# Performance work log

Hardware: AMD Instinct MI355X
Metric: run time of the kernel (lower is better)

## Reference

```python
import jax, jax.numpy as jnp
import numpy as np

B, T, N, H = 512, 128, 128, 256


def setup_inputs() -> dict:
    key = jax.random.key(0)
    ks = jax.random.split(key, 8)
    rn = lambda k, shape, sc: (jax.random.normal(k, shape, jnp.float32) * sc)
    return {
        "data": rn(ks[0], (B, T, N), 1.0),
        "h0": jnp.zeros((B, H), jnp.float32),
        # SimpleRNNCell params: h_t = tanh(x@Wx + h@Wh + b)
        "Wx": rn(ks[1], (N, H), 0.05),
        "Wh": rn(ks[2], (H, H), 0.05),
        "b": jnp.zeros((H,), jnp.float32),
        # InputAttention: w1: Dense(T) over last dim T; w2: Dense(T) over hidden; v: Dense(1)
        "W1": rn(ks[3], (T, T), 0.05),
        "b1": jnp.zeros((T,), jnp.float32),
        "W2": rn(ks[4], (H, T), 0.05),
        "b2": jnp.zeros((T,), jnp.float32),
        "Wv": rn(ks[5], (T, 1), 0.05),
        "bv": jnp.zeros((1,), jnp.float32),
        "n": N,
    }


def reference(data, h0, Wx, Wh, b, W1, b1, W2, b2, Wv, bv, n):
    # data: (B, T, n); h0: (B, H)
    Tlen = data.shape[1]
    x_perm = jnp.swapaxes(data, 1, 2)          # (B, n, T) == Permute((2,1))(x)
    pre = x_perm @ W1 + b1                      # w1(x_perm): loop-invariant, hoisted

    def step(h, x_t):
        # SimpleRNNCell: new state used for this step's attention
        h_new = jnp.tanh(x_t @ Wx + h @ Wh + b)                 # (B, H)
        q = h_new @ W2 + b2                                      # w2(RepeatVector(n)(h)) per row -> (B, T)
        score = jnp.tanh(pre + q[:, None, :])                    # (B, n, T)
        e = score @ Wv + bv                                      # (B, n, 1)
        e = jnp.swapaxes(e, 1, 2)                                # Permute((2,1)) -> (B, 1, n)
        alpha = jax.nn.softmax(e, axis=-1)                       # softmax over n
        return h_new, alpha

    xs = jnp.swapaxes(data, 0, 1)               # (T, B, n): data[:, t, :] per step
    _, alphas = jax.lax.scan(step, h0, xs)      # (T, B, 1, n)
    # faithful to tf.reshape(alpha_seq.stack(), (-1, T, n))
    alpha_seq = alphas.reshape(-1, Tlen, n)     # (B, T, n)
    return data * alpha_seq
```

## Files before the change

kernel.cpp:

```cpp
#include <hip/hip_runtime.h>


#define C2L 2.8853900817779268f
#define L2E 1.4426950408889634f

typedef _Float16 hf;
typedef _Float16 hf2 __attribute__((ext_vector_type(2)));
typedef _Float16 hf4 __attribute__((ext_vector_type(4)));
typedef _Float16 hf8 __attribute__((ext_vector_type(8)));
typedef float f32x4 __attribute__((ext_vector_type(4)));

__device__ __forceinline__ float fast_exp2(float x){
#if __has_builtin(__builtin_amdgcn_exp2f)
  return __builtin_amdgcn_exp2f(x);
#else
  return exp2f(x);
#endif
}
__device__ __forceinline__ float fast_rcp(float x){
#if __has_builtin(__builtin_amdgcn_rcpf)
  return __builtin_amdgcn_rcpf(x);
#else
  return 1.f/x;
#endif
}

__global__ __launch_bounds__(256) void k_prep_w(const float* __restrict__ Wx,
    const float* __restrict__ W2, const float* __restrict__ W1,
    hf* __restrict__ wts){
  int tid = blockIdx.x*256 + threadIdx.x;
  if (tid < 32768){
    int n = tid >> 7, k = tid & 127;
    wts[tid] = (hf)Wx[k*256 + n];
  } else if (tid < 65536){
    int t2 = tid - 32768;
    int n = t2 >> 8, k = t2 & 255;
    wts[tid] = (hf)W2[k*128 + n];
  } else {
    int t3 = tid - 65536;
    int n = t3 >> 7, k = t3 & 127;
    wts[tid] = (hf)W1[k*128 + n];
  }
}

template<int K, int MODE>
__global__ __launch_bounds__(256) void k_gemm(const void* __restrict__ Asrc,
    const hf* __restrict__ Bt, const float* __restrict__ bias,
    float* __restrict__ Cout){
  constexpr int SA = 136;
  __shared__ alignas(16) hf As[64*SA];
  __shared__ alignas(16) hf Bs[128*SA];
  const int tid = threadIdx.x;
  const int w = tid >> 6, lane = tid & 63;
  const int c = lane & 15, q = lane >> 4;
  const int bx = blockIdx.x;
  const int col0 = (MODE==0) ? blockIdx.y*128 : 0;

  float br[8];
  #pragma unroll
  for (int ni=0; ni<8; ni++) br[ni] = bias[col0 + ni*16 + c];

  f32x4 acc[8];
  #pragma unroll
  for (int ni=0; ni<8; ni++) acc[ni] = (f32x4){0.f,0.f,0.f,0.f};

  for (int kc=0; kc<K/128; kc++){
    if (MODE == 0){
      const float* A = (const float*)Asrc + (long)bx*64*128;
      #pragma unroll
      for (int v=0; v<8; v++){
        int f4 = v*256 + tid;
        int m = f4 >> 5, k4 = (f4 & 31)*4;
        float4 d = *(const float4*)&A[m*128 + k4];
        hf4 h = {(hf)d.x,(hf)d.y,(hf)d.z,(hf)d.w};
        *(hf4*)&As[m*SA + k4] = h;
      }
    } else if (MODE == 1){
      const hf* A = (const hf*)Asrc + (long)bx*64*256;
      #pragma unroll
      for (int v=0; v<4; v++){
        int f8 = v*256 + tid;
        int m = f8 >> 4, k8 = (f8 & 15)*8;
        *(hf8*)&As[m*SA + k8] = *(const hf8*)&A[m*256 + kc*128 + k8];
      }
    } else {
      const float* A = (const float*)Asrc + (long)(bx>>1)*16384;
      const int i0 = (bx & 1)*64;
      #pragma unroll
      for (int v=0; v<8; v++){
        int f4 = v*256 + tid;
        int t = f4 >> 4, i4 = (f4 & 15)*4;
        float4 d = *(const float4*)&A[t*128 + i0 + i4];
        As[(i4+0)*SA + t] = (hf)d.x;
        As[(i4+1)*SA + t] = (hf)d.y;
        As[(i4+2)*SA + t] = (hf)d.z;
        As[(i4+3)*SA + t] = (hf)d.w;
      }
    }
    #pragma unroll
    for (int v=0; v<8; v++){
      int f8 = v*256 + tid;
      int n = f8 >> 4, k8 = (f8 & 15)*8;
      *(hf8*)&Bs[n*SA + k8] = *(const hf8*)&Bt[(col0+n)*K + kc*128 + k8];
    }
    __syncthreads();
    #pragma unroll
    for (int kk=0; kk<4; kk++){
      hf8 a = *(const hf8*)&As[(w*16 + c)*SA + kk*32 + q*8];
      #pragma unroll
      for (int ni=0; ni<8; ni++){
        hf8 b = *(const hf8*)&Bs[(ni*16 + c)*SA + kk*32 + q*8];
        acc[ni] = __builtin_amdgcn_mfma_f32_16x16x32_f16(a, b, acc[ni], 0, 0, 0);
      }
    }
    __syncthreads();
  }
  #pragma unroll
  for (int ni=0; ni<8; ni++){
    #pragma unroll
    for (int r=0; r<4; r++){
      int rloc = w*16 + q*4 + r;
      int col = col0 + ni*16 + c;
      float val = acc[ni][r] + br[ni];
      int addr;
      if (MODE == 0){
        int R = bx*64 + rloc;
        int b_ = R >> 7, t_ = R & 127;
        addr = (t_*512 + b_)*256 + col;
      } else if (MODE == 1){
        int R = bx*64 + rloc;
        addr = R*128 + col;
        val = fast_exp2(C2L*val);
      } else {
        int b_ = bx >> 1, i_ = (bx & 1)*64 + rloc;
        addr = b_*16384 + i_*128 + col;
        val = fast_exp2(C2L*val);
      }
      Cout[addr] = val;
    }
  }
}

__global__ __launch_bounds__(512, 2) void k_rnn(const float* __restrict__ h0,
    const float* __restrict__ Wh, const float* __restrict__ xw,
    hf* __restrict__ Hb){
  __shared__ alignas(16) char hs[2*8192];
  const int tid = threadIdx.x;
  const int w = tid >> 6, lane = tid & 63;
  const int c = lane & 15, q = lane >> 4;
  const int b0 = blockIdx.x * 16;
  const int w0 = w * 32;
  hf8 bw[2][8];
  #pragma unroll
  for (int nt=0; nt<2; nt++){
    #pragma unroll
    for (int kc=0; kc<8; kc++){
      #pragma unroll
      for (int e=0; e<8; e++){
        bw[nt][kc][e] = (hf)Wh[(kc*32 + q*8 + e)*256 + w0 + nt*16 + c];
      }
    }
  }
  {
    int m = tid >> 5, s8 = tid & 31;
    const float* src = &h0[(b0 + m)*256 + s8*8];
    float4 d0 = *(const float4*)&src[0];
    float4 d1 = *(const float4*)&src[4];
    hf8 hv = {(hf)d0.x,(hf)d0.y,(hf)d0.z,(hf)d0.w,
              (hf)d1.x,(hf)d1.y,(hf)d1.z,(hf)d1.w};
    *(hf8*)&hs[m*512 + ((s8 ^ (m & 7)) << 4)] = hv;
  }
  float xwv[2][4];
  #pragma unroll
  for (int nt=0; nt<2; nt++){
    #pragma unroll
    for (int r=0; r<4; r++)
      xwv[nt][r] = xw[(b0 + q*4 + r)*256 + w0 + nt*16 + c];
  }
  __syncthreads();
  const int m = c;
  const int abase = m*512;
  for (int t=0; t<128; t++){
    const int p = t & 1;
    float xwn[2][4];
    if (t < 127){
      #pragma unroll
      for (int nt=0; nt<2; nt++){
        #pragma unroll
        for (int r=0; r<4; r++)
          xwn[nt][r] = xw[((t+1)*512 + b0 + q*4 + r)*256 + w0 + nt*16 + c];
      }
    } else {
      #pragma unroll
      for (int nt=0; nt<2; nt++){
        #pragma unroll
        for (int r=0; r<4; r++) xwn[nt][r] = 0.f;
      }
    }
    hf8 a[8];
    #pragma unroll
    for (int kc=0; kc<8; kc++)
      a[kc] = *(const hf8*)&hs[p*8192 + abase + ((((kc<<2)|q) ^ (m & 7)) << 4)];
    f32x4 acc0 = (f32x4){0.f,0.f,0.f,0.f};
    f32x4 acc1 = (f32x4){0.f,0.f,0.f,0.f};
    #pragma unroll
    for (int kc=0; kc<8; kc++){
      acc0 = __builtin_amdgcn_mfma_f32_16x16x32_f16(a[kc], bw[0][kc], acc0, 0,0,0);
      acc1 = __builtin_amdgcn_mfma_f32_16x16x32_f16(a[kc], bw[1][kc], acc1, 0,0,0);
    }
    #pragma unroll
    for (int nt=0; nt<2; nt++){
      #pragma unroll
      for (int r=0; r<4; r++){
        float v = (nt ? acc1[r] : acc0[r]) + xwv[nt][r];
        float e2 = fast_exp2(v*C2L);
        float hn = 1.f - 2.f*fast_rcp(e2 + 1.f);
        int row = q*4 + r;
        int col = w0 + nt*16 + c;
        *(hf*)&hs[(p^1)*8192 + row*512
                  + (((col >> 3) ^ (row & 7)) << 4) + (col & 7)*2] = (hf)hn;
        Hb[(t*512 + b0 + row)*256 + col] = (hf)hn;
        xwv[nt][r] = xwn[nt][r];
      }
    }
    __syncthreads();
  }
}

__global__ __launch_bounds__(256, 4) void k_attn(const float* __restrict__ P,
    const float* __restrict__ Qm, const float* __restrict__ Wv,
    const float* __restrict__ data, float* __restrict__ out){
  __shared__ alignas(16) float qs[32*128];
  __shared__ alignas(16) float wvs[128];
  __shared__ alignas(16) float epart[2][2][4][128];
  __shared__ float red[2][4][2];
  const int b = blockIdx.x, tile = blockIdx.y;
  const int tid = threadIdx.x;
  const int i = tid & 127, hl = tid >> 7;
  const int t0 = tile*32;
  if (tid < 128) wvs[tid] = -2.f*Wv[tid];
  #pragma unroll
  for (int v=0; v<4; v++){
    int flat = v*1024 + tid*4;
    int tt = flat >> 7, c = flat & 127;
    *(float4*)&qs[flat] = *(const float4*)&Qm[((t0+tt)*512 + b)*128 + c];
  }
  float4 p4[16];
  const float* prow = P + b*16384 + i*128 + hl*64;
  #pragma unroll
  for (int v=0; v<16; v++) p4[v] = *(const float4*)&prow[v*4];
  __syncthreads();
  for (int tp=0; tp<8; tp++){
    const int pp = tp & 1;
    const float* q0r = &qs[(4*tp)*128   + hl*64];
    const float* q1r = &qs[(4*tp+1)*128 + hl*64];
    const float* q2r = &qs[(4*tp+2)*128 + hl*64];
    const float* q3r = &qs[(4*tp+3)*128 + hl*64];
    const float* wvr = &wvs[hl*64];
    float acc0=0.f, acc1=0.f, acc2=0.f, acc3=0.f;
    #pragma unroll
    for (int m=0; m<16; m++){
      float4 Pv = p4[m];
      float4 wv = *(const float4*)&wvr[m*4];
      {
        float4 qq = *(const float4*)&q0r[m*4];
        float u = fmaf(Pv.x, qq.x, 1.f), v = fmaf(Pv.y, qq.y, 1.f);
        float n = fmaf(wv.x, v, wv.y*u);
        acc0 = fmaf(n, fast_rcp(u*v), acc0);
        float u2 = fmaf(Pv.z, qq.z, 1.f), v2 = fmaf(Pv.w, qq.w, 1.f);
        float n2 = fmaf(wv.z, v2, wv.w*u2);
        acc0 = fmaf(n2, fast_rcp(u2*v2), acc0);
      }
      {
        float4 qq = *(const float4*)&q1r[m*4];
        float u = fmaf(Pv.x, qq.x, 1.f), v = fmaf(Pv.y, qq.y, 1.f);
        float n = fmaf(wv.x, v, wv.y*u);
        acc1 = fmaf(n, fast_rcp(u*v), acc1);
        float u2 = fmaf(Pv.z, qq.z, 1.f), v2 = fmaf(Pv.w, qq.w, 1.f);
        float n2 = fmaf(wv.z, v2, wv.w*u2);
        acc1 = fmaf(n2, fast_rcp(u2*v2), acc1);
      }
      {
        float4 qq = *(const float4*)&q2r[m*4];
        float u = fmaf(Pv.x, qq.x, 1.f), v = fmaf(Pv.y, qq.y, 1.f);
        float n = fmaf(wv.x, v, wv.y*u);
        acc2 = fmaf(n, fast_rcp(u*v), acc2);
        float u2 = fmaf(Pv.z, qq.z, 1.f), v2 = fmaf(Pv.w, qq.w, 1.f);
        float n2 = fmaf(wv.z, v2, wv.w*u2);
        acc2 = fmaf(n2, fast_rcp(u2*v2), acc2);
      }
      {
        float4 qq = *(const float4*)&q3r[m*4];
        float u = fmaf(Pv.x, qq.x, 1.f), v = fmaf(Pv.y, qq.y, 1.f);
        float n = fmaf(wv.x, v, wv.y*u);
        acc3 = fmaf(n, fast_rcp(u*v), acc3);
        float u2 = fmaf(Pv.z, qq.z, 1.f), v2 = fmaf(Pv.w, qq.w, 1.f);
        float n2 = fmaf(wv.z, v2, wv.w*u2);
        acc3 = fmaf(n2, fast_rcp(u2*v2), acc3);
      }
    }
    epart[pp][hl][0][i] = acc0;
    epart[pp][hl][1][i] = acc1;
    epart[pp][hl][2][i] = acc2;
    epart[pp][hl][3][i] = acc3;
    __syncthreads();
    const int g = tid >> 7;
    float pe[2];
    #pragma unroll
    for (int s=0; s<2; s++){
      int tl = g + 2*s;
      float e = epart[pp][0][tl][i] + epart[pp][1][tl][i];
      pe[s] = fast_exp2(e*L2E);
      float sm = pe[s];
      #pragma unroll
      for (int off=32; off; off>>=1) sm += __shfl_xor(sm, off);
      if ((tid & 63) == 0) red[pp][tl][(tid>>6)&1] = sm;
    }
    __syncthreads();
    #pragma unroll
    for (int s=0; s<2; s++){
      int tl = g + 2*s;
      float ssum = red[pp][tl][0] + red[pp][tl][1];
      float alpha = pe[s] * fast_rcp(ssum);
      int t = t0 + 4*tp + tl;
      int base = (t*512 + b)*128 + i;
      out[base] = data[base]*alpha;
    }
  }
}

extern "C" void kernel_launch(void* const* d_in, const int* in_sizes, int n_in,
                              void* d_out, int out_size, void* d_ws, size_t ws_size,
                              hipStream_t stream) {
  const float* data = (const float*)d_in[0];
  const float* h0   = (const float*)d_in[1];
  const float* Wx   = (const float*)d_in[2];
  const float* Wh   = (const float*)d_in[3];
  const float* bb   = (const float*)d_in[4];
  const float* W1   = (const float*)d_in[5];
  const float* b1   = (const float*)d_in[6];
  const float* W2   = (const float*)d_in[7];
  const float* b2   = (const float*)d_in[8];
  const float* Wv   = (const float*)d_in[9];
  float* wsp = (float*)d_ws;
  float* P   = wsp;
  float* xwQ = wsp + 8388608;
  hf*    Hbf = (hf*)(wsp + 25165824);
  hf*    wts = (hf*)(wsp + 33554432);
  const hf* Wxt = wts;
  const hf* W2t = wts + 32768;
  const hf* W1t = wts + 65536;
  float* out = (float*)d_out;

  hipLaunchKernelGGL(k_prep_w, dim3(320), dim3(256), 0, stream, Wx, W2, W1, wts);
  hipLaunchKernelGGL((k_gemm<128,0>), dim3(1024,2), dim3(256), 0, stream,
                     (const void*)data, Wxt, bb, xwQ);
  hipLaunchKernelGGL((k_gemm<128,2>), dim3(1024),   dim3(256), 0, stream,
                     (const void*)data, W1t, b1, P);
  hipLaunchKernelGGL(k_rnn, dim3(32), dim3(512), 0, stream, h0, Wh, xwQ, Hbf);
  hipLaunchKernelGGL((k_gemm<256,1>), dim3(1024),   dim3(256), 0, stream,
                     (const void*)Hbf, W2t, b2, xwQ);
  hipLaunchKernelGGL(k_attn, dim3(512, 4), dim3(256), 0, stream, P, xwQ, Wv, data, out);
}
```

Measured before the change: 372.7 us.

## Double thread counts in RNN and attention kernels and merge reciprocals

The serial RNN kernel moves from 512 to 1024 threads per block, so each wave owns one 16-column tile and splits its K reduction into two independent MFMA chains, which shortens the per-step critical path. The attention kernel moves to 512 threads, each handling a quarter of the hidden dimension instead of half, and combines pairs of reciprocals into a single rcp per four elements. The cost is more per-block partial sums to reduce through LDS, higher register pressure under the new launch bounds, and some extra rounding risk from the merged reciprocal.

New measurement: 354.2 us. 1.05x faster.

```diff
diff --git a/kernel.cpp b/kernel.cpp
--- a/kernel.cpp
+++ b/kernel.cpp
@@ -141,7 +141,7 @@
   }
 }
 
-__global__ __launch_bounds__(512, 2) void k_rnn(const float* __restrict__ h0,
+__global__ __launch_bounds__(1024, 4) void k_rnn(const float* __restrict__ h0,
     const float* __restrict__ Wh, const float* __restrict__ xw,
     hf* __restrict__ Hb){
   __shared__ alignas(16) char hs[2*8192];
@@ -149,19 +149,16 @@
   const int w = tid >> 6, lane = tid & 63;
   const int c = lane & 15, q = lane >> 4;
   const int b0 = blockIdx.x * 16;
-  const int w0 = w * 32;
-  hf8 bw[2][8];
-  #pragma unroll
-  for (int nt=0; nt<2; nt++){
-    #pragma unroll
-    for (int kc=0; kc<8; kc++){
-      #pragma unroll
-      for (int e=0; e<8; e++){
-        bw[nt][kc][e] = (hf)Wh[(kc*32 + q*8 + e)*256 + w0 + nt*16 + c];
-      }
-    }
-  }
-  {
+  const int col = w*16 + c;
+  hf8 bw[8];
+  #pragma unroll
+  for (int kc=0; kc<8; kc++){
+    #pragma unroll
+    for (int e=0; e<8; e++){
+      bw[kc][e] = (hf)Wh[(kc*32 + q*8 + e)*256 + col];
+    }
+  }
+  if (tid < 512){
     int m = tid >> 5, s8 = tid & 31;
     const float* src = &h0[(b0 + m)*256 + s8*8];
     float4 d0 = *(const float4*)&src[0];
@@ -170,162 +167,115 @@
               (hf)d1.x,(hf)d1.y,(hf)d1.z,(hf)d1.w};
     *(hf8*)&hs[m*512 + ((s8 ^ (m & 7)) << 4)] = hv;
   }
-  float xwv[2][4];
-  #pragma unroll
-  for (int nt=0; nt<2; nt++){
-    #pragma unroll
-    for (int r=0; r<4; r++)
-      xwv[nt][r] = xw[(b0 + q*4 + r)*256 + w0 + nt*16 + c];
-  }
+  float xwv[4];
+  #pragma unroll
+  for (int r=0; r<4; r++) xwv[r] = xw[(b0 + q*4 + r)*256 + col];
   __syncthreads();
   const int m = c;
   const int abase = m*512;
   for (int t=0; t<128; t++){
     const int p = t & 1;
-    float xwn[2][4];
+    float xwn[4];
     if (t < 127){
       #pragma unroll
-      for (int nt=0; nt<2; nt++){
-        #pragma unroll
-        for (int r=0; r<4; r++)
-          xwn[nt][r] = xw[((t+1)*512 + b0 + q*4 + r)*256 + w0 + nt*16 + c];
-      }
+      for (int r=0; r<4; r++) xwn[r] = xw[((t+1)*512 + b0 + q*4 + r)*256 + col];
     } else {
       #pragma unroll
-      for (int nt=0; nt<2; nt++){
-        #pragma unroll
-        for (int r=0; r<4; r++) xwn[nt][r] = 0.f;
-      }
+      for (int r=0; r<4; r++) xwn[r] = 0.f;
     }
     hf8 a[8];
     #pragma unroll
     for (int kc=0; kc<8; kc++)
       a[kc] = *(const hf8*)&hs[p*8192 + abase + ((((kc<<2)|q) ^ (m & 7)) << 4)];
-    f32x4 acc0 = (f32x4){0.f,0.f,0.f,0.f};
-    f32x4 acc1 = (f32x4){0.f,0.f,0.f,0.f};
-    #pragma unroll
-    for (int kc=0; kc<8; kc++){
-      acc0 = __builtin_amdgcn_mfma_f32_16x16x32_f16(a[kc], bw[0][kc], acc0, 0,0,0);
-      acc1 = __builtin_amdgcn_mfma_f32_16x16x32_f16(a[kc], bw[1][kc], acc1, 0,0,0);
-    }
-    #pragma unroll
-    for (int nt=0; nt<2; nt++){
-      #pragma unroll
-      for (int r=0; r<4; r++){
-        float v = (nt ? acc1[r] : acc0[r]) + xwv[nt][r];
-        float e2 = fast_exp2(v*C2L);
-        float hn = 1.f - 2.f*fast_rcp(e2 + 1.f);
-        int row = q*4 + r;
-        int col = w0 + nt*16 + c;
-        *(hf*)&hs[(p^1)*8192 + row*512
-                  + (((col >> 3) ^ (row & 7)) << 4) + (col & 7)*2] = (hf)hn;
-        Hb[(t*512 + b0 + row)*256 + col] = (hf)hn;
-        xwv[nt][r] = xwn[nt][r];
-      }
-    }
-    __syncthreads();
-  }
-}
-
-__global__ __launch_bounds__(256, 4) void k_attn(const float* __restrict__ P,
+    f32x4 acca = (f32x4){0.f,0.f,0.f,0.f};
+    f32x4 accb = (f32x4){0.f,0.f,0.f,0.f};
+    #pragma unroll
+    for (int kc=0; kc<4; kc++){
+      acca = __builtin_amdgcn_mfma_f32_16x16x32_f16(a[kc],   bw[kc],   acca, 0,0,0);
+      accb = __builtin_amdgcn_mfma_f32_16x16x32_f16(a[kc+4], bw[kc+4], accb, 0,0,0);
+    }
+    #pragma unroll
+    for (int r=0; r<4; r++){
+      float v = acca[r] + accb[r] + xwv[r];
+      float e2 = fast_exp2(v*C2L);
+      float hn = 1.f - 2.f*fast_rcp(e2 + 1.f);
+      int row = q*4 + r;
+      *(hf*)&hs[(p^1)*8192 + row*512
+                + (((col >> 3) ^ (row & 7)) << 4) + (col & 7)*2] = (hf)hn;
+      Hb[(t*512 + b0 + row)*256 + col] = (hf)hn;
+      xwv[r] = xwn[r];
+    }
+    __syncthreads();
+  }
+}
+
+__global__ __launch_bounds__(512, 4) void k_attn(const float* __restrict__ P,
     const float* __restrict__ Qm, const float* __restrict__ Wv,
     const float* __restrict__ data, float* __restrict__ out){
   __shared__ alignas(16) float qs[32*128];
   __shared__ alignas(16) float wvs[128];
-  __shared__ alignas(16) float epart[2][2][4][128];
+  __shared__ alignas(16) float epart[2][4][4][128];
   __shared__ float red[2][4][2];
   const int b = blockIdx.x, tile = blockIdx.y;
   const int tid = threadIdx.x;
-  const int i = tid & 127, hl = tid >> 7;
+  const int i = tid & 127, g = tid >> 7;
   const int t0 = tile*32;
   if (tid < 128) wvs[tid] = -2.f*Wv[tid];
   #pragma unroll
-  for (int v=0; v<4; v++){
-    int flat = v*1024 + tid*4;
+  for (int v=0; v<2; v++){
+    int flat = v*2048 + tid*4;
     int tt = flat >> 7, c = flat & 127;
     *(float4*)&qs[flat] = *(const float4*)&Qm[((t0+tt)*512 + b)*128 + c];
   }
-  float4 p4[16];
-  const float* prow = P + b*16384 + i*128 + hl*64;
-  #pragma unroll
-  for (int v=0; v<16; v++) p4[v] = *(const float4*)&prow[v*4];
+  float4 p4[8];
+  const float* prow = P + b*16384 + i*128 + g*32;
+  #pragma unroll
+  for (int v=0; v<8; v++) p4[v] = *(const float4*)&prow[v*4];
   __syncthreads();
   for (int tp=0; tp<8; tp++){
     const int pp = tp & 1;
-    const float* q0r = &qs[(4*tp)*128   + hl*64];
-    const float* q1r = &qs[(4*tp+1)*128 + hl*64];
-    const float* q2r = &qs[(4*tp+2)*128 + hl*64];
-    const float* q3r = &qs[(4*tp+3)*128 + hl*64];
-    const float* wvr = &wvs[hl*64];
+    const float* qb  = &qs[(4*tp)*128 + g*32];
+    const float* wvr = &wvs[g*32];
     float acc0=0.f, acc1=0.f, acc2=0.f, acc3=0.f;
     #pragma unroll
-    for (int m=0; m<16; m++){
-      float4 Pv = p4[m];
-      float4 wv = *(const float4*)&wvr[m*4];
-      {
-        float4 qq = *(const float4*)&q0r[m*4];
+    for (int mm=0; mm<8; mm++){
+      float4 Pv = p4[mm];
+      float4 wv = *(const float4*)&wvr[mm*4];
+      #pragma unroll
+      for (int tl=0; tl<4; tl++){
+        float4 qq = *(const float4*)&qb[tl*128 + mm*4];
         float u = fmaf(Pv.x, qq.x, 1.f), v = fmaf(Pv.y, qq.y, 1.f);
-        float n = fmaf(wv.x, v, wv.y*u);
-        acc0 = fmaf(n, fast_rcp(u*v), acc0);
-        float u2 = fmaf(Pv.z, qq.z, 1.f), v2 = fmaf(Pv.w, qq.w, 1.f);
-        float n2 = fmaf(wv.z, v2, wv.w*u2);
-        acc0 = fmaf(n2, fast_rcp(u2*v2), acc0);
-      }
-      {
-        float4 qq = *(const float4*)&q1r[m*4];
-        float u = fmaf(Pv.x, qq.x, 1.f), v = fmaf(Pv.y, qq.y, 1.f);
-        float n = fmaf(wv.x, v, wv.y*u);
-        acc1 = fmaf(n, fast_rcp(u*v), acc1);
-        float u2 = fmaf(Pv.z, qq.z, 1.f), v2 = fmaf(Pv.w, qq.w, 1.f);
-        float n2 = fmaf(wv.z, v2, wv.w*u2);
-        acc1 = fmaf(n2, fast_rcp(u2*v2), acc1);
-      }
-      {
-        float4 qq = *(const float4*)&q2r[m*4];
-        float u = fmaf(Pv.x, qq.x, 1.f), v = fmaf(Pv.y, qq.y, 1.f);
-        float n = fmaf(wv.x, v, wv.y*u);
-        acc2 = fmaf(n, fast_rcp(u*v), acc2);
-        float u2 = fmaf(Pv.z, qq.z, 1.f), v2 = fmaf(Pv.w, qq.w, 1.f);
-        float n2 = fmaf(wv.z, v2, wv.w*u2);
-        acc2 = fmaf(n2, fast_rcp(u2*v2), acc2);
-      }
-      {
-        float4 qq = *(const float4*)&q3r[m*4];
-        float u = fmaf(Pv.x, qq.x, 1.f), v = fmaf(Pv.y, qq.y, 1.f);
-        float n = fmaf(wv.x, v, wv.y*u);
-        acc3 = fmaf(n, fast_rcp(u*v), acc3);
-        float u2 = fmaf(Pv.z, qq.z, 1.f), v2 = fmaf(Pv.w, qq.w, 1.f);
-        float n2 = fmaf(wv.z, v2, wv.w*u2);
-        acc3 = fmaf(n2, fast_rcp(u2*v2), acc3);
-      }
-    }
-    epart[pp][hl][0][i] = acc0;
-    epart[pp][hl][1][i] = acc1;
-    epart[pp][hl][2][i] = acc2;
-    epart[pp][hl][3][i] = acc3;
-    __syncthreads();
-    const int g = tid >> 7;
-    float pe[2];
-    #pragma unroll
-    for (int s=0; s<2; s++){
-      int tl = g + 2*s;
-      float e = epart[pp][0][tl][i] + epart[pp][1][tl][i];
-      pe[s] = fast_exp2(e*L2E);
-      float sm = pe[s];
-      #pragma unroll
-      for (int off=32; off; off>>=1) sm += __shfl_xor(sm, off);
-      if ((tid & 63) == 0) red[pp][tl][(tid>>6)&1] = sm;
-    }
-    __syncthreads();
-    #pragma unroll
-    for (int s=0; s<2; s++){
-      int tl = g + 2*s;
-      float ssum = red[pp][tl][0] + red[pp][tl][1];
-      float alpha = pe[s] * fast_rcp(ssum);
-      int t = t0 + 4*tp + tl;
-      int base = (t*512 + b)*128 + i;
-      out[base] = data[base]*alpha;
-    }
+        float x = fmaf(Pv.z, qq.z, 1.f), y = fmaf(Pv.w, qq.w, 1.f);
+        float d01 = u*v, d23 = x*y;
+        float n01 = fmaf(wv.x, v, wv.y*u);
+        float n23 = fmaf(wv.z, y, wv.w*x);
+        float N = fmaf(n01, d23, n23*d01);
+        float r = fast_rcp(d01*d23);
+        float term = N*r;
+        if (tl==0) acc0 += term;
+        else if (tl==1) acc1 += term;
+        else if (tl==2) acc2 += term;
+        else acc3 += term;
+      }
+    }
+    epart[pp][g][0][i] = acc0;
+    epart[pp][g][1][i] = acc1;
+    epart[pp][g][2][i] = acc2;
+    epart[pp][g][3][i] = acc3;
+    __syncthreads();
+    float e = epart[pp][0][g][i] + epart[pp][1][g][i]
+            + epart[pp][2][g][i] + epart[pp][3][g][i];
+    float pe = fast_exp2(e*L2E);
+    float sm = pe;
+    #pragma unroll
+    for (int off=32; off; off>>=1) sm += __shfl_xor(sm, off);
+    if ((tid & 63) == 0) red[pp][g][(tid>>6)&1] = sm;
+    __syncthreads();
+    float ssum = red[pp][g][0] + red[pp][g][1];
+    float alpha = pe * fast_rcp(ssum);
+    int t = t0 + 4*tp + g;
+    int base = (t*512 + b)*128 + i;
+    out[base] = data[base]*alpha;
   }
 }
 
@@ -357,8 +307,8 @@
                      (const void*)data, Wxt, bb, xwQ);
   hipLaunchKernelGGL((k_gemm<128,2>), dim3(1024),   dim3(256), 0, stream,
                      (const void*)data, W1t, b1, P);
-  hipLaunchKernelGGL(k_rnn, dim3(32), dim3(512), 0, stream, h0, Wh, xwQ, Hbf);
+  hipLaunchKernelGGL(k_rnn, dim3(32), dim3(1024), 0, stream, h0, Wh, xwQ, Hbf);
   hipLaunchKernelGGL((k_gemm<256,1>), dim3(1024),   dim3(256), 0, stream,
                      (const void*)Hbf, W2t, b2, xwQ);
-  hipLaunchKernelGGL(k_attn, dim3(512, 4), dim3(256), 0, stream, P, xwQ, Wv, data, out);
-}
+  hipLaunchKernelGGL(k_attn, dim3(512, 4), dim3(512), 0, stream, P, xwQ, Wv, data, out);
+}
```
